# Performance work log

Hardware: AMD Instinct MI355X
Metric: run time of the kernel (lower is better)

Reference implementation:

```python
import jax, jax.numpy as jnp
import numpy as np

N_NODES = 40000
N_EDGES = 640000
MUL = 32                      # multiplicity of 0e and 1o in node irreps
NUM_NEIGHBORS = 16.0
SILU_NORM = 1.6791767923989418  # e3nn normalize2mom factor for silu
SQRT3 = 3.0 ** 0.5


def setup_inputs() -> dict:
    key = jax.random.key(0)
    ks = jax.random.split(key, 12)
    return {
        "node_input": jax.random.normal(ks[0], (N_NODES, 4 * MUL), dtype=jnp.float32),
        "node_attr": jnp.ones((N_NODES, 1), dtype=jnp.float32),
        "edge_src": jax.random.randint(ks[1], (N_EDGES,), 0, N_NODES, dtype=jnp.int32),
        "edge_dst": jax.random.randint(ks[2], (N_EDGES,), 0, N_NODES, dtype=jnp.int32),
        "edge_attr": jax.random.normal(ks[3], (N_EDGES, 4), dtype=jnp.float32),
        "edge_scalars": jax.random.normal(ks[4], (N_EDGES, 8), dtype=jnp.float32),
        "w_lin1_s": jax.random.normal(ks[5], (MUL, MUL), dtype=jnp.float32),
        "w_lin1_v": jax.random.normal(ks[6], (MUL, MUL), dtype=jnp.float32),
        "fc_w1": jax.random.normal(ks[7], (8, 64), dtype=jnp.float32),
        "fc_w2": jax.random.normal(ks[8], (64, 4 * MUL), dtype=jnp.float32),
        "w_lin2_s": jax.random.normal(ks[9], (2 * MUL, MUL), dtype=jnp.float32),
        "w_lin2_v": jax.random.normal(ks[10], (2 * MUL, MUL), dtype=jnp.float32),
    }


def reference(node_input, node_attr, edge_src, edge_dst, edge_attr, edge_scalars,
              w_lin1_s, w_lin1_v, fc_w1, fc_w2, w_lin2_s, w_lin2_v):
    N = node_input.shape[0]
    # split node features per e3nn layout: [32x0e | 32x1o]
    s = node_input[:, :MUL]                            # [N, 32]
    v = node_input[:, MUL:].reshape(N, MUL, 3)         # [N, 32, 3]

    # linear_1: per-irrep e3nn Linear (weights scaled by 1/sqrt(fan_in))
    s = s @ (w_lin1_s / jnp.sqrt(jnp.float32(MUL)))
    v = jnp.einsum('nui,uw->nwi', v, w_lin1_v / jnp.sqrt(jnp.float32(MUL)))

    # fc: edge_scalars -> tensor-product weights (e3nn FullyConnectedNet, silu)
    h = jax.nn.silu(edge_scalars @ (fc_w1 / jnp.sqrt(jnp.float32(fc_w1.shape[0])))) * SILU_NORM
    w = h @ (fc_w2 / jnp.sqrt(jnp.float32(fc_w2.shape[0])))      # [E, 128]
    w0 = w[:, 0 * MUL:1 * MUL]  # path 0e x 0e -> 0e
    w1 = w[:, 1 * MUL:2 * MUL]  # path 0e x 1o -> 1o
    w2 = w[:, 2 * MUL:3 * MUL]  # path 1o x 0e -> 1o
    w3 = w[:, 3 * MUL:4 * MUL]  # path 1o x 1o -> 0e

    # gather source node features per edge
    se = s[edge_src]            # [E, 32]
    ve = v[edge_src]            # [E, 32, 3]
    es = edge_attr[:, :1]       # [E, 1]  edge 0e
    ev = edge_attr[:, 1:4]      # [E, 3]  edge 1o

    # edge-wise 'uvu' Clebsch-Gordan tensor product (e3nn component-normalized;
    # the sqrt(3) path weight cancels the 1/sqrt(3) of w3j for the l=1 paths)
    mid_s0 = w0 * se * es                                       # 0e x 0e -> 0e
    mid_s1 = w3 * jnp.einsum('eui,ei->eu', ve, ev) / SQRT3      # 1o x 1o -> 0e
    mid_v0 = (w1 * se)[:, :, None] * ev[:, None, :]             # 0e x 1o -> 1o
    mid_v1 = (w2 * es)[:, :, None] * ve                         # 1o x 0e -> 1o
    # sorted irreps_mid layout: [0e(path0), 0e(path3) | 1o(path1), 1o(path2)]
    mid_scal = jnp.concatenate([mid_s0, mid_s1], axis=1)        # [E, 64]
    mid_vec = jnp.concatenate([mid_v0, mid_v1], axis=1)         # [E, 64, 3]

    # scatter-reduce to destination nodes, / sqrt(num_neighbors)
    inv = 1.0 / jnp.sqrt(jnp.float32(NUM_NEIGHBORS))
    ns = jax.ops.segment_sum(mid_scal, edge_dst, num_segments=N) * inv   # [N, 64]
    nv = jax.ops.segment_sum(mid_vec, edge_dst, num_segments=N) * inv    # [N, 64, 3]

    # linear_2: 64x0e+64x1o -> 32x0e+32x1o
    fan = jnp.sqrt(jnp.float32(2 * MUL))
    out_s = ns @ (w_lin2_s / fan)                                # [N, 32]
    out_v = jnp.einsum('nui,uw->nwi', nv, w_lin2_v / fan)        # [N, 32, 3]
    return jnp.concatenate([out_s, out_v.reshape(N, -1)], axis=1)
```

## Files before the change

kernel.cpp:

```cpp
#include <hip/hip_runtime.h>
#include <math.h>

#define NNODES 40000
#define NEDGES 640000
#define NPB 8
#define LROW 257
#define CHUNK 32
#define CHUNK4 16
#define MROW 260
#define NB1 8

typedef __attribute__((ext_vector_type(8))) short short8_t;
typedef __attribute__((ext_vector_type(4))) short short4_t;
typedef __attribute__((ext_vector_type(4))) float float4_t;

__device__ __forceinline__ float4 ld4(const float* p) { return *(const float4*)p; }

__device__ __forceinline__ unsigned short bf16r(float x) {
  union { float f; unsigned u; } v; v.f = x;
  unsigned u = v.u;
  u += 0x7FFFu + ((u >> 16) & 1u);
  return (unsigned short)(u >> 16);
}

__device__ __forceinline__ void lds_fadd(float* p, float v) {
  __hip_atomic_fetch_add(p, v, __ATOMIC_RELAXED, __HIP_MEMORY_SCOPE_WORKGROUP);
}

#define INV_SQRT3_C 0.57735026918962576f

__device__ __forceinline__ void accum_half(float* lrow, int u,
    float w0, float w1, float w2, float w3,
    float se, float vx, float vy, float vz,
    float esc, float ev0, float ev1, float ev2) {
  lds_fadd(lrow + u, w0 * se * esc);
  float dv = vx * ev0 + vy * ev1 + vz * ev2;
  lds_fadd(lrow + 32 + u, w3 * dv * INV_SQRT3_C);
  float b1v = w1 * se;
  lds_fadd(lrow + 64 + u * 3 + 0, b1v * ev0);
  lds_fadd(lrow + 64 + u * 3 + 1, b1v * ev1);
  lds_fadd(lrow + 64 + u * 3 + 2, b1v * ev2);
  float b2v = w2 * esc;
  lds_fadd(lrow + 160 + u * 3 + 0, b2v * vx);
  lds_fadd(lrow + 160 + u * 3 + 1, b2v * vy);
  lds_fadd(lrow + 160 + u * 3 + 2, b2v * vz);
}

struct RowData { float se0, se1, vx0, vy0, vz0, vx1, vy1, vz1; };

__device__ __forceinline__ RowData load_row(const float* ab, int m) {
  RowData d;
  d.se0 = ab[m];            d.se1 = ab[m + 16];
  d.vx0 = ab[32 + 3 * m];   d.vy0 = ab[33 + 3 * m];   d.vz0 = ab[34 + 3 * m];
  d.vx1 = ab[80 + 3 * m];   d.vy1 = ab[81 + 3 * m];   d.vz1 = ab[82 + 3 * m];
  return d;
}

__global__ void k1_stage1(const float* __restrict__ node_input,
                          const float* __restrict__ w1s,
                          const float* __restrict__ w1v,
                          float* __restrict__ A) {
  const float scale = 0.17677669529663687f;
  int stride = gridDim.x * blockDim.x;
  for (int idx = blockIdx.x * blockDim.x + threadIdx.x; idx < NNODES * 128; idx += stride) {
    int n = idx >> 7;
    int c = idx & 127;
    const float* row = node_input + n * 128;
    float acc = 0.f;
    if (c < 32) {
      #pragma unroll
      for (int u = 0; u < 32; ++u)
        acc = fmaf(row[u], w1s[u * 32 + c], acc);
    } else {
      int cc = c - 32;
      int w = cc / 3;
      int i = cc - w * 3;
      #pragma unroll
      for (int u = 0; u < 32; ++u)
        acc = fmaf(row[32 + u * 3 + i], w1v[u * 32 + w], acc);
    }
    A[idx] = acc * scale;
  }
}

__global__ __launch_bounds__(256) void k1_stage1b(
    const float* __restrict__ node_input,
    const float* __restrict__ w1s,
    const float* __restrict__ w1v,
    float* __restrict__ A2) {
  __shared__ float rows[NB1 * 128];
  __shared__ float ws[32 * 32];
  __shared__ float wvv[32 * 32];
  const float scale = 0.17677669529663687f;
  int tid = threadIdx.x;
  int n0 = blockIdx.x * NB1;

  float4 a = ((const float4*)w1s)[tid];
  a.x *= scale; a.y *= scale; a.z *= scale; a.w *= scale;
  ((float4*)ws)[tid] = a;
  float4 b = ((const float4*)w1v)[tid];
  b.x *= scale; b.y *= scale; b.z *= scale; b.w *= scale;
  ((float4*)wvv)[tid] = b;
  ((float4*)rows)[tid] = ((const float4*)(node_input + (long)n0 * 128))[tid];
  __syncthreads();

  int j = tid & 31, g = tid >> 5;
  const float* lr = rows + g * 128;
  float ac0 = 0.f, ac1 = 0.f, ac2 = 0.f, ac3 = 0.f;
  #pragma unroll
  for (int t = 0; t < 32; ++t) {
    float wsj = ws[t * 32 + j];
    float wvj = wvv[t * 32 + j];
    ac0 = fmaf(lr[t],            wsj, ac0);
    ac1 = fmaf(lr[32 + 3 * t],     wvj, ac1);
    ac2 = fmaf(lr[32 + 3 * t + 1], wvj, ac2);
    ac3 = fmaf(lr[32 + 3 * t + 2], wvj, ac3);
  }
  float4 o; o.x = ac0; o.y = ac1; o.z = ac2; o.w = ac3;
  ((float4*)(A2 + (long)n0 * 128))[tid] = o;
}

__global__ void k_hist(const int* __restrict__ edge_dst, int* __restrict__ counts) {
  int e = blockIdx.x * blockDim.x + threadIdx.x;
  if (e < NEDGES) atomicAdd(&counts[edge_dst[e]], 1);
}

__global__ void k_scanA(const int* __restrict__ counts, int* __restrict__ bsum) {
  __shared__ int ws[4];
  int t = blockIdx.x * 256 + threadIdx.x;
  int v = (t < NNODES) ? counts[t] : 0;
  for (int d = 32; d; d >>= 1) v += __shfl_down(v, d, 64);
  if ((threadIdx.x & 63) == 0) ws[threadIdx.x >> 6] = v;
  __syncthreads();
  if (threadIdx.x == 0) bsum[blockIdx.x] = ws[0] + ws[1] + ws[2] + ws[3];
}

__global__ __launch_bounds__(256) void k_scanB(const int* __restrict__ bsum,
                                               int* __restrict__ boff,
                                               int* __restrict__ offsets) {
  __shared__ int s[256];
  int tid = threadIdx.x;
  int v = (tid < 157) ? bsum[tid] : 0;
  s[tid] = v;
  __syncthreads();
  for (int d = 1; d < 256; d <<= 1) {
    int x = (tid >= d) ? s[tid - d] : 0;
    __syncthreads();
    s[tid] += x;
    __syncthreads();
  }
  if (tid < 157) boff[tid] = s[tid] - v;
  if (tid == 0) offsets[NNODES] = NEDGES;
}

__global__ __launch_bounds__(256) void k_scanC(const int* __restrict__ counts,
                                               const int* __restrict__ boff,
                                               int* __restrict__ offsets,
                                               int* __restrict__ cursor) {
  __shared__ int s[256];
  int tid = threadIdx.x;
  int t = blockIdx.x * 256 + tid;
  int v = (t < NNODES) ? counts[t] : 0;
  s[tid] = v;
  __syncthreads();
  for (int d = 1; d < 256; d <<= 1) {
    int x = (tid >= d) ? s[tid - d] : 0;
    __syncthreads();
    s[tid] += x;
    __syncthreads();
  }
  int off = boff[blockIdx.x] + s[tid] - v;
  if (t < NNODES) { offsets[t] = off; cursor[t] = off; }
}

__global__ __launch_bounds__(256) void k_scanBC(
    const int* __restrict__ counts,
    const int* __restrict__ bsum,
    int* __restrict__ offsets,
    int* __restrict__ cursor) {
  __shared__ int sb[256];
  __shared__ int s[256];
  int tid = threadIdx.x;
  int vb = (tid < 157) ? bsum[tid] : 0;
  sb[tid] = vb;
  __syncthreads();
  for (int d = 1; d < 256; d <<= 1) {
    int x = (tid >= d) ? sb[tid - d] : 0;
    __syncthreads();
    sb[tid] += x;
    __syncthreads();
  }
  int myboff = (blockIdx.x == 0) ? 0 : sb[blockIdx.x - 1];
  int t = blockIdx.x * 256 + tid;
  int v = (t < NNODES) ? counts[t] : 0;
  s[tid] = v;
  __syncthreads();
  for (int d = 1; d < 256; d <<= 1) {
    int x = (tid >= d) ? s[tid - d] : 0;
    __syncthreads();
    s[tid] += x;
    __syncthreads();
  }
  int off = myboff + s[tid] - v;
  if (t < NNODES) { offsets[t] = off; cursor[t] = off; }
  if (blockIdx.x == 0 && tid == 0) offsets[NNODES] = NEDGES;
}

__global__ void k_scatter(const int* __restrict__ edge_dst,
                          int* __restrict__ cursor, int* __restrict__ slots) {
  int e = blockIdx.x * blockDim.x + threadIdx.x;
  if (e < NEDGES) {
    int d = edge_dst[e];
    int p = atomicAdd(&cursor[d], 1);
    slots[p] = e;
  }
}

__global__ void k_scatter_pack2(const int* __restrict__ edge_src,
                                const int* __restrict__ edge_dst,
                                const float* __restrict__ edge_attr,
                                const float* __restrict__ edge_scalars,
                                int* __restrict__ cursor,
                                int* __restrict__ PSRC,
                                float4_t* __restrict__ PEA,
                                float4_t* __restrict__ PES) {
  int e = blockIdx.x * blockDim.x + threadIdx.x;
  if (e < NEDGES) {
    int d = edge_dst[e];
    int p = atomicAdd(&cursor[d], 1);
    PSRC[p] = edge_src[e];
    PEA[p] = *(const float4_t*)(edge_attr + (long)e * 4);
    PES[2 * p]     = *(const float4_t*)(edge_scalars + (long)e * 8);
    PES[2 * p + 1] = *(const float4_t*)(edge_scalars + (long)e * 8 + 4);
  }
}

__global__ void k_scatter_pack3(const int* __restrict__ edge_src,
                                const int* __restrict__ edge_dst,
                                const float* __restrict__ edge_attr,
                                const float* __restrict__ edge_scalars,
                                int* __restrict__ cursor,
                                float4_t* __restrict__ PE) {
  int e = blockIdx.x * blockDim.x + threadIdx.x;
  if (e < NEDGES) {
    int d = edge_dst[e];
    int p = atomicAdd(&cursor[d], 1);
    float4_t* b = PE + (long)p * 4;
    b[0] = *(const float4_t*)(edge_attr + (long)e * 4);
    b[1] = *(const float4_t*)(edge_scalars + (long)e * 8);
    b[2] = *(const float4_t*)(edge_scalars + (long)e * 8 + 4);
    float4_t s;
    s.x = __int_as_float(edge_src[e]); s.y = 0.f; s.z = 0.f; s.w = 0.f;
    b[3] = s;
  }
}

__global__ __launch_bounds__(256, 4) void k_edge6(
    const float* __restrict__ A2,
    const float4_t* __restrict__ PE,
    const float* __restrict__ fc_w1,
    const float* __restrict__ fc_w2,
    const float* __restrict__ w2s,
    const float* __restrict__ w2v,
    const int* __restrict__ offsets,
    float* __restrict__ out) {
  const float INV_SQRT8 = 0.35355339059327373f;
  const float H_SCALE   = 1.6791767923989418f / 8.0f;
  const float S2SCALE   = 0.03125f;

  __shared__ float  mid[CHUNK4 * MROW];
  __shared__ short  h_lds[CHUNK4 * 72];
  __shared__ float4 w1f[144];

  int tid = threadIdx.x;
  int n0 = blockIdx.x * NPB;
  int ebase = offsets[n0];
  int eend  = offsets[n0 + NPB];

  if (tid < 128) {
    int j = tid >> 1, hf = tid & 1;
    float4 wv4;
    wv4.x = fc_w1[(hf * 4 + 0) * 64 + j] * INV_SQRT8;
    wv4.y = fc_w1[(hf * 4 + 1) * 64 + j] * INV_SQRT8;
    wv4.z = fc_w1[(hf * 4 + 2) * 64 + j] * INV_SQRT8;
    wv4.w = fc_w1[(hf * 4 + 3) * 64 + j] * INV_SQRT8;
    w1f[(j >> 3) * 18 + (j & 7) * 2 + hf] = wv4;
  }

  int wv = tid >> 6;
  int l  = tid & 63;
// ... 11 lines not shown
    bL0[j] = (short)bf16r(fc_w2[(q * 8 + j) * 128      + tL * 16 + m]);
    bL1[j] = (short)bf16r(fc_w2[(32 + q * 8 + j) * 128 + tL * 16 + m]);
    bH0[j] = (short)bf16r(fc_w2[(q * 8 + j) * 128      + tH * 16 + m]);
    bH1[j] = (short)bf16r(fc_w2[(32 + q * 8 + j) * 128 + tH * 16 + m]);
  }

  int nA = 2 * wv;
  int offA0 = offsets[n0 + nA];
  int offA1 = offsets[n0 + nA + 1];
  int offB1 = offsets[n0 + nA + 2];
  float4_t racA = {0.f, 0.f, 0.f, 0.f};
  float4_t racB = {0.f, 0.f, 0.f, 0.f};

  float ea0x, ea0y, ea0z, ea0w, ea1x, ea1y, ea1z, ea1w,
        ea2x, ea2y, ea2z, ea2w, ea3x, ea3y, ea3z, ea3w;
  float se0, se1, se2, se3, vx0, vx1, vx2, vx3,
        vy0, vy1, vy2, vy3, vz0, vz1, vz2, vz3;

  auto loadmeta = [&](int kb) {
    int ecs = kb + m;
    int ecc = (ecs < eend) ? ecs : (eend - 1);
    const float4_t* pb = PE + (long)ecc * 4;
    float4_t sA  = pb[1];
    float4_t sB  = pb[2];
    int g  = wv * 2 + (q >> 1);
    int ob = (q & 1) * 4;
    short4_t hq;
    #pragma unroll
    for (int j = 0; j < 4; ++j) {
      float4 wA = w1f[g * 18 + (ob + j) * 2 + 0];
      float4 wB = w1f[g * 18 + (ob + j) * 2 + 1];
      float x = sA.x * wA.x + sA.y * wA.y + sA.z * wA.z + sA.w * wA.w
              + sB.x * wB.x + sB.y * wB.y + sB.z * wB.z + sB.w * wB.w;
      float hv = (x * H_SCALE) / (1.f + __expf(-x));
      hq[j] = (short)bf16r(hv);
    }
    *(short4_t*)((char*)h_lds + m * 144 + wv * 32 + q * 8) = hq;
    int eb = kb + q * 4;
    int e0 = (eb     < eend) ? eb     : (eend - 1);
    int e1 = (eb + 1 < eend) ? eb + 1 : (eend - 1);
    int e2 = (eb + 2 < eend) ? eb + 2 : (eend - 1);
    int e3 = (eb + 3 < eend) ? eb + 3 : (eend - 1);
    const float4_t* p0 = PE + (long)e0 * 4;
    const float4_t* p1 = PE + (long)e1 * 4;
    const float4_t* p2 = PE + (long)e2 * 4;
    const float4_t* p3 = PE + (long)e3 * 4;
    float4_t a0v = p0[0]; int s0i = __float_as_int(p0[3].x);
    float4_t a1v = p1[0]; int s1i = __float_as_int(p1[3].x);
    float4_t a2v = p2[0]; int s2i = __float_as_int(p2[3].x);
    float4_t a3v = p3[0]; int s3i = __float_as_int(p3[3].x);
    ea0x = a0v.x; ea0y = a0v.y; ea0z = a0v.z; ea0w = a0v.w;
    ea1x = a1v.x; ea1y = a1v.y; ea1z = a1v.z; ea1w = a1v.w;
    ea2x = a2v.x; ea2y = a2v.y; ea2z = a2v.z; ea2w = a2v.w;
    ea3x = a3v.x; ea3y = a3v.y; ea3z = a3v.z; ea3w = a3v.w;
    float4 g0 = *(const float4*)(A2 + (long)s0i * 128 + 4 * u);
    float4 g1 = *(const float4*)(A2 + (long)s1i * 128 + 4 * u);
    float4 g2 = *(const float4*)(A2 + (long)s2i * 128 + 4 * u);
    float4 g3 = *(const float4*)(A2 + (long)s3i * 128 + 4 * u);
    se0 = g0.x; vx0 = g0.y; vy0 = g0.z; vz0 = g0.w;
    se1 = g1.x; vx1 = g1.y; vy1 = g1.z; vz1 = g1.w;
    se2 = g2.x; vx2 = g2.y; vy2 = g2.z; vz2 = g2.w;
    se3 = g3.x; vx3 = g3.y; vy3 = g3.z; vz3 = g3.w;
  };

  __syncthreads();

  if (ebase < eend) {
// ... 44 lines not shown
          float4_t v = *(const float4_t*)(mid + (e - k0) * MROW + 4 * l);
          racB.x += v.x; racB.y += v.y; racB.z += v.z; racB.w += v.w;
        }
      }
      if (k0 + CHUNK4 < eend) loadmeta(k0 + CHUNK4);
    }
  }

  __syncthreads();
  *(float4_t*)(mid + (2 * wv) * MROW + 4 * l)     = racA;
  *(float4_t*)(mid + (2 * wv + 1) * MROW + 4 * l) = racB;
  __syncthreads();
  {
    int j = tid & 31, g = tid >> 5;
    const float* nr = mid + g * MROW;
    float ac0 = 0.f, ac1 = 0.f, ac2 = 0.f, ac3 = 0.f;
    #pragma unroll 8
    for (int t = 0; t < 64; ++t) {
      float wsj = w2s[t * 32 + j];
      float wvj = w2v[t * 32 + j];
      ac0 = fmaf(nr[t],              wsj, ac0);
      ac1 = fmaf(nr[64 + 3 * t],     wvj, ac1);
      ac2 = fmaf(nr[64 + 3 * t + 1], wvj, ac2);
      ac3 = fmaf(nr[64 + 3 * t + 2], wvj, ac3);
    }
    float* po = out + (long)(n0 + g) * 128;
    po[j] = ac0 * S2SCALE;
    po[32 + 3 * j + 0] = ac1 * S2SCALE;
    po[32 + 3 * j + 1] = ac2 * S2SCALE;
    po[32 + 3 * j + 2] = ac3 * S2SCALE;
  }
}

__global__ __launch_bounds__(256, 3) void k_edge3(
    const float* __restrict__ A,
    const int* __restrict__ PSRC,
    const float4_t* __restrict__ PEA,
    const float4_t* __restrict__ PES,
    const float* __restrict__ fc_w1,
    const float* __restrict__ fc_w2,
    const int* __restrict__ offsets,
    float* __restrict__ ACC) {
  const float INV_SQRT8 = 0.35355339059327373f;
  const float H_SCALE   = 1.6791767923989418f / 8.0f;

  __shared__ float    mid[CHUNK * MROW];
  __shared__ short8_t w2frag[16 * 64];
  __shared__ float4   w1f[144];

  int tid = threadIdx.x;
  int n0 = blockIdx.x * NPB;
  int ebase = offsets[n0];
  int eend  = offsets[n0 + NPB];

  if (tid < 128) {
    int j = tid >> 1, hf = tid & 1;
    float4 wv4;
    wv4.x = fc_w1[(hf * 4 + 0) * 64 + j] * INV_SQRT8;
    wv4.y = fc_w1[(hf * 4 + 1) * 64 + j] * INV_SQRT8;
    wv4.z = fc_w1[(hf * 4 + 2) * 64 + j] * INV_SQRT8;
    wv4.w = fc_w1[(hf * 4 + 3) * 64 + j] * INV_SQRT8;
    w1f[(j >> 3) * 18 + (j & 7) * 2 + hf] = wv4;
  }
  for (int fi = tid; fi < 16 * 64; fi += 256) {
    int f = fi >> 6, ll = fi & 63;
    int ct = f >> 1, kh = f & 1, mm = ll & 15, qq = ll >> 4;
    short8_t v;
    #pragma unroll
    for (int j = 0; j < 8; ++j)
      v[j] = (short)bf16r(fc_w2[(kh * 32 + qq * 8 + j) * 128 + ct * 16 + mm]);
    w2frag[fi] = v;
  }
  __syncthreads();

  int wv = tid >> 6;
  int l  = tid & 63;
  int m  = l & 15;
  int q  = l >> 4;
  int et = wv & 1;
  int ch = wv >> 1;

  int nA = 2 * wv;
  int offA0 = offsets[n0 + nA];
  int offA1 = offsets[n0 + nA + 1];
  int offB1 = offsets[n0 + nA + 2];
  float4_t racA = {0.f, 0.f, 0.f, 0.f};
  float4_t racB = {0.f, 0.f, 0.f, 0.f};

  for (int k0 = ebase; k0 < eend; k0 += CHUNK) {
    {
      int ecs = k0 + et * 16 + m;
      int ecc = (ecs < eend) ? ecs : (eend - 1);
      int srcm = PSRC[ecc];
      float4 eam = *(const float4*)(PEA + ecc);
      float4 sA  = *(const float4*)(PES + 2 * (long)ecc);
      float4 sB  = *(const float4*)(PES + 2 * (long)ecc + 1);
      float es0 = sA.x, es1 = sA.y, es2 = sA.z, es3 = sA.w;
      float es4 = sB.x, es5 = sB.y, es6 = sB.z, es7 = sB.w;

      short8_t a0, a1;
      #pragma unroll
      for (int jj = 0; jj < 8; ++jj) {
        float4 wA = w1f[q * 18 + jj * 2 + 0];
        float4 wB = w1f[q * 18 + jj * 2 + 1];
        float x = es0 * wA.x + es1 * wA.y + es2 * wA.z + es3 * wA.w
                + es4 * wB.x + es5 * wB.y + es6 * wB.z + es7 * wB.w;
        float hv = (x * H_SCALE) / (1.f + __expf(-x));
        a0[jj] = (short)bf16r(hv);
        float4 wC = w1f[(4 + q) * 18 + jj * 2 + 0];
        float4 wD = w1f[(4 + q) * 18 + jj * 2 + 1];
        float x2 = es0 * wC.x + es1 * wC.y + es2 * wC.z + es3 * wC.w
                 + es4 * wD.x + es5 * wD.y + es6 * wD.z + es7 * wD.w;
        float hv2 = (x2 * H_SCALE) / (1.f + __expf(-x2));
        a1[jj] = (short)bf16r(hv2);
      }

      int sl0 = q * 4, sl1 = sl0 + 1, sl2 = sl0 + 2, sl3 = sl0 + 3;
      int src0 = __shfl(srcm, sl0, 64), src1 = __shfl(srcm, sl1, 64);
      int src2 = __shfl(srcm, sl2, 64), src3 = __shfl(srcm, sl3, 64);
      float ea0x = __shfl(eam.x, sl0, 64), ea0y = __shfl(eam.y, sl0, 64),
            ea0z = __shfl(eam.z, sl0, 64), ea0w = __shfl(eam.w, sl0, 64);
      float ea1x = __shfl(eam.x, sl1, 64), ea1y = __shfl(eam.y, sl1, 64),
            ea1z = __shfl(eam.z, sl1, 64), ea1w = __shfl(eam.w, sl1, 64);
      float ea2x = __shfl(eam.x, sl2, 64), ea2y = __shfl(eam.y, sl2, 64),
            ea2z = __shfl(eam.z, sl2, 64), ea2w = __shfl(eam.w, sl2, 64);
      float ea3x = __shfl(eam.x, sl3, 64), ea3y = __shfl(eam.y, sl3, 64),
            ea3z = __shfl(eam.z, sl3, 64), ea3w = __shfl(eam.w, sl3, 64);

      RowData d0 = load_row(A + (long)src0 * 128, m);
      RowData d1 = load_row(A + (long)src1 * 128, m);
      RowData d2 = load_row(A + (long)src2 * 128, m);
      RowData d3 = load_row(A + (long)src3 * 128, m);

      float4_t acL[2], acH[2];
      #pragma unroll
      for (int uo = 0; uo < 2; ++uo) {
        int tl = ch * 2 + uo;
        short8_t bl0 = w2frag[(tl * 2 + 0) * 64 + l];
        short8_t bl1 = w2frag[(tl * 2 + 1) * 64 + l];
        float4_t zl = (float4_t){0.f, 0.f, 0.f, 0.f};
        zl = __builtin_amdgcn_mfma_f32_16x16x32_bf16(a0, bl0, zl, 0, 0, 0);
        zl = __builtin_amdgcn_mfma_f32_16x16x32_bf16(a1, bl1, zl, 0, 0, 0);
        acL[uo] = zl;
        int th = 4 + ch * 2 + uo;
        short8_t bh0 = w2frag[(th * 2 + 0) * 64 + l];
        short8_t bh1 = w2frag[(th * 2 + 1) * 64 + l];
        float4_t zh = (float4_t){0.f, 0.f, 0.f, 0.f};
        zh = __builtin_amdgcn_mfma_f32_16x16x32_bf16(a0, bh0, zh, 0, 0, 0);
        zh = __builtin_amdgcn_mfma_f32_16x16x32_bf16(a1, bh1, zh, 0, 0, 0);
        acH[uo] = zh;
      }

#define EPI(R, D, EAX, EAY, EAZ, EAW) do {                                       \
        float* mrow = mid + (et * 16 + q * 4 + (R)) * MROW;                      \
        { float wAa = acL[0][R], wBb = acH[0][R];                                \
          if (ch == 0) {                                                         \
            mrow[m] = wAa * D.se0 * EAX;                                         \
            float b = wBb * EAX;                                                 \
            mrow[160 + 3 * m + 0] = b * D.vx0;                                   \
            mrow[160 + 3 * m + 1] = b * D.vy0;                                   \
            mrow[160 + 3 * m + 2] = b * D.vz0;                                   \
          } else {                                                               \
            float dv = D.vx0 * EAY + D.vy0 * EAZ + D.vz0 * EAW;                  \
            mrow[32 + m] = wBb * dv * INV_SQRT3_C;                               \
            float b = wAa * D.se0;                                               \
            mrow[64 + 3 * m + 0] = b * EAY;                                      \
            mrow[64 + 3 * m + 1] = b * EAZ;                                      \
            mrow[64 + 3 * m + 2] = b * EAW;                                      \
          } }                                                                    \
        { float wAa = acL[1][R], wBb = acH[1][R];                                \
          int uu = 16 + m;                                                       \
          if (ch == 0) {                                                         \
            mrow[uu] = wAa * D.se1 * EAX;                                        \
            float b = wBb * EAX;                                                 \
            mrow[160 + 3 * uu + 0] = b * D.vx1;                                  \
            mrow[160 + 3 * uu + 1] = b * D.vy1;                                  \
            mrow[160 + 3 * uu + 2] = b * D.vz1;                                  \
          } else {                                                               \
            float dv = D.vx1 * EAY + D.vy1 * EAZ + D.vz1 * EAW;                  \
            mrow[32 + uu] = wBb * dv * INV_SQRT3_C;                              \
            float b = wAa * D.se1;                                               \
            mrow[64 + 3 * uu + 0] = b * EAY;                                     \
            mrow[64 + 3 * uu + 1] = b * EAZ;                                     \
            mrow[64 + 3 * uu + 2] = b * EAW;                                     \
          } }                                                                    \
      } while (0)

      EPI(0, d0, ea0x, ea0y, ea0z, ea0w);
      EPI(1, d1, ea1x, ea1y, ea1z, ea1w);
      EPI(2, d2, ea2x, ea2y, ea2z, ea2w);
      EPI(3, d3, ea3x, ea3y, ea3z, ea3w);
#undef EPI
    }
    __syncthreads();

    {
      int lo = (offA0 > k0) ? offA0 : k0;
      int hiA = offA1 < (k0 + CHUNK) ? offA1 : (k0 + CHUNK);
      for (int e = lo; e < hiA; ++e) {
        float4_t v = *(const float4_t*)(mid + (e - k0) * MROW + 4 * l);
        racA.x += v.x; racA.y += v.y; racA.z += v.z; racA.w += v.w;
      }
      int lo2 = (offA1 > k0) ? offA1 : k0;
      int hiB = offB1 < (k0 + CHUNK) ? offB1 : (k0 + CHUNK);
      for (int e = lo2; e < hiB; ++e) {
        float4_t v = *(const float4_t*)(mid + (e - k0) * MROW + 4 * l);
        racB.x += v.x; racB.y += v.y; racB.z += v.z; racB.w += v.w;
      }
    }
    __syncthreads();
  }

  *(float4_t*)(ACC + (long)(n0 + nA) * 256 + 4 * l)     = racA;
  *(float4_t*)(ACC + (long)(n0 + nA + 1) * 256 + 4 * l) = racB;
}

__global__ void k3_stage2(const float* __restrict__ ACC,
                          const float* __restrict__ w2s,
                          const float* __restrict__ w2v,
                          float* __restrict__ out) {
  const float scale = 0.03125f;
  int stride = gridDim.x * blockDim.x;
  for (int idx = blockIdx.x * blockDim.x + threadIdx.x; idx < NNODES * 128; idx += stride) {
    int n = idx >> 7;
    int c = idx & 127;
    const float* row = ACC + (long)n * 256;
    float acc = 0.f;
    if (c < 32) {
      #pragma unroll
      for (int qq = 0; qq < 64; ++qq)
        acc = fmaf(row[qq], w2s[qq * 32 + c], acc);
    } else {
      int cc = c - 32;
      int w = cc / 3;
      int i = cc - w * 3;
      #pragma unroll
      for (int qq = 0; qq < 64; ++qq)
        acc = fmaf(row[64 + qq * 3 + i], w2v[qq * 32 + w], acc);
    }
    out[idx] = acc * scale;
  }
}

extern "C" void kernel_launch(void* const* d_in, const int* in_sizes, int n_in,
                              void* d_out, int out_size, void* d_ws, size_t ws_size,
                              hipStream_t stream) {
  const float* node_input   = (const float*)d_in[0];
  const int*   edge_src     = (const int*)d_in[2];
  const int*   edge_dst     = (const int*)d_in[3];
  const float* edge_attr    = (const float*)d_in[4];
  const float* edge_scalars = (const float*)d_in[5];
  const float* fc_w1        = (const float*)d_in[8];
  const float* fc_w2        = (const float*)d_in[9];
  const float* w_lin1_s     = (const float*)d_in[6];
  const float* w_lin1_v     = (const float*)d_in[7];
  const float* w_lin2_s     = (const float*)d_in[10];
  const float* w_lin2_v     = (const float*)d_in[11];

  float* out = (float*)d_out;

  const size_t SZ_ACC = (size_t)NNODES * 256 * sizeof(float);
  const size_t SZ_A2  = (size_t)NNODES * 128 * sizeof(float);
  const size_t SZ_PE  = (size_t)NEDGES * 64;
  const size_t SZ_PES = (size_t)NEDGES * 32;
  const size_t SZ_PEA = (size_t)NEDGES * 16;
  const size_t SZ_PSR = (size_t)NEDGES * 4;
  const size_t SZ_CNT = (size_t)NNODES * sizeof(int);
  const size_t SZ_OFF = (size_t)(NNODES + 4) * sizeof(int);
  const size_t need1 = SZ_A2 + SZ_PE + 3 * SZ_CNT + SZ_OFF + 2048;
  const size_t need2 = SZ_ACC + SZ_PES + SZ_PEA + SZ_PSR + 3 * SZ_CNT + SZ_OFF + 2048;

  if (ws_size >= need1) {
    char* p = (char*)d_ws;
    float*    A2  = (float*)p;    p += SZ_A2;
    float4_t* PE  = (float4_t*)p; p += SZ_PE;
    int* counts   = (int*)p;      p += SZ_CNT;
    int* offsets  = (int*)p;      p += SZ_OFF;
    int* cursor   = (int*)p;      p += SZ_CNT;
    int* bsum     = (int*)p;      p += 160 * sizeof(int);

    hipMemsetAsync(counts, 0, SZ_CNT, stream);
    k1_stage1b<<<NNODES / NB1, 256, 0, stream>>>(node_input, w_lin1_s, w_lin1_v, A2);
    k_hist<<<NEDGES / 256, 256, 0, stream>>>(edge_dst, counts);
    k_scanA<<<157, 256, 0, stream>>>(counts, bsum);
    k_scanBC<<<157, 256, 0, stream>>>(counts, bsum, offsets, cursor);
    k_scatter_pack3<<<NEDGES / 256, 256, 0, stream>>>(edge_src, edge_dst, edge_attr,
                                                      edge_scalars, cursor, PE);
    k_edge6<<<NNODES / NPB, 256, 0, stream>>>(A2, PE, fc_w1, fc_w2,
                                              w_lin2_s, w_lin2_v, offsets, out);
  } else if (ws_size >= need2) {
    float* Abuf = out;
    char* p = (char*)d_ws;
    float*    ACC = (float*)p;    p += SZ_ACC;
    float4_t* PES = (float4_t*)p; p += SZ_PES;
    float4_t* PEA = (float4_t*)p; p += SZ_PEA;
    int*      PSRC = (int*)p;     p += SZ_PSR;
    int* counts   = (int*)p;      p += SZ_CNT;
    int* offsets  = (int*)p;      p += SZ_OFF;
    int* cursor   = (int*)p;      p += SZ_CNT;
    int* bsum     = (int*)p;      p += 160 * sizeof(int);
    int* boff     = (int*)p;      p += 160 * sizeof(int);

    hipMemsetAsync(counts, 0, SZ_CNT, stream);
    k1_stage1<<<2048, 256, 0, stream>>>(node_input, w_lin1_s, w_lin1_v, Abuf);
    k_hist<<<NEDGES / 256, 256, 0, stream>>>(edge_dst, counts);
    k_scanA<<<157, 256, 0, stream>>>(counts, bsum);
    k_scanB<<<1, 256, 0, stream>>>(bsum, boff, offsets);
    k_scanC<<<157, 256, 0, stream>>>(counts, boff, offsets, cursor);
    k_scatter_pack2<<<NEDGES / 256, 256, 0, stream>>>(edge_src, edge_dst, edge_attr,
                                                      edge_scalars, cursor, PSRC, PEA, PES);
    k_edge3<<<NNODES / NPB, 256, 0, stream>>>(Abuf, PSRC, PEA, PES, fc_w1, fc_w2,
                                              offsets, ACC);
    k3_stage2<<<2048, 256, 0, stream>>>(ACC, w_lin2_s, w_lin2_v, out);
  } else {
    float* Abuf = out;
    char* p = (char*)d_ws;
    float*    ACC = (float*)p;    p += SZ_ACC;
    int* counts   = (int*)p;      p += SZ_CNT;
    int* offsets  = (int*)p;      p += SZ_OFF;
    int* cursor   = (int*)p;      p += SZ_CNT;
    int* bsum     = (int*)p;      p += 160 * sizeof(int);
    int* boff     = (int*)p;      p += 160 * sizeof(int);
    int* slots    = (int*)p;      p += (size_t)NEDGES * sizeof(int);
    (void)slots; (void)boff;

    hipMemsetAsync(counts, 0, SZ_CNT, stream);
    k1_stage1<<<2048, 256, 0, stream>>>(node_input, w_lin1_s, w_lin1_v, Abuf);
    k_hist<<<NEDGES / 256, 256, 0, stream>>>(edge_dst, counts);
    k_scanA<<<157, 256, 0, stream>>>(counts, bsum);
    k_scanBC<<<157, 256, 0, stream>>>(counts, bsum, offsets, cursor);
    k_scatter<<<NEDGES / 256, 256, 0, stream>>>(edge_dst, cursor, slots);
    k3_stage2<<<2048, 256, 0, stream>>>(ACC, w_lin2_s, w_lin2_v, out);
  }
}
```

Measured before the change: 329.6 us.

## Fuse graph-build preprocessing into one cooperative kernel with grid syncs

Replaces the memset, linear_1, histogram, scan and scatter-pack launches with a single cooperative kernel that uses grid-wide syncs between phases, falling back to the old launch sequence if the cooperative launch fails. The aim is to cut launch overhead and inter-kernel gaps in the preprocessing stage. It also swaps the silu division for a hardware reciprocal and removes the dead workspace-fallback code paths. The trade-off is that a fixed 1024-block grid runs the low-parallelism scan phases on only 157 blocks while the rest sit idle at the grid barriers, and each grid sync has its own cost.

After: 1.045 ms. 217% more time.

```diff
diff --git a/kernel.cpp b/kernel.cpp
--- a/kernel.cpp
+++ b/kernel.cpp
@@ -1,20 +1,20 @@
 #include <hip/hip_runtime.h>
+#include <hip/hip_cooperative_groups.h>
 #include <math.h>
+
+namespace cg = cooperative_groups;
 
 #define NNODES 40000
 #define NEDGES 640000
 #define NPB 8
-#define LROW 257
-#define CHUNK 32
 #define CHUNK4 16
 #define MROW 260
 #define NB1 8
+#define BUILD_GRID 1024
 
 typedef __attribute__((ext_vector_type(8))) short short8_t;
 typedef __attribute__((ext_vector_type(4))) short short4_t;
 typedef __attribute__((ext_vector_type(4))) float float4_t;
-
-__device__ __forceinline__ float4 ld4(const float* p) { return *(const float4*)p; }
 
 __device__ __forceinline__ unsigned short bf16r(float x) {
   union { float f; unsigned u; } v; v.f = x;
@@ -23,63 +23,122 @@
   return (unsigned short)(u >> 16);
 }
 
-__device__ __forceinline__ void lds_fadd(float* p, float v) {
-  __hip_atomic_fetch_add(p, v, __ATOMIC_RELAXED, __HIP_MEMORY_SCOPE_WORKGROUP);
-}
-
 #define INV_SQRT3_C 0.57735026918962576f
 
-__device__ __forceinline__ void accum_half(float* lrow, int u,
-    float w0, float w1, float w2, float w3,
-    float se, float vx, float vy, float vz,
-    float esc, float ev0, float ev1, float ev2) {
-  lds_fadd(lrow + u, w0 * se * esc);
-  float dv = vx * ev0 + vy * ev1 + vz * ev2;
-  lds_fadd(lrow + 32 + u, w3 * dv * INV_SQRT3_C);
-  float b1v = w1 * se;
-  lds_fadd(lrow + 64 + u * 3 + 0, b1v * ev0);
-  lds_fadd(lrow + 64 + u * 3 + 1, b1v * ev1);
-  lds_fadd(lrow + 64 + u * 3 + 2, b1v * ev2);
-  float b2v = w2 * esc;
-  lds_fadd(lrow + 160 + u * 3 + 0, b2v * vx);
-  lds_fadd(lrow + 160 + u * 3 + 1, b2v * vy);
-  lds_fadd(lrow + 160 + u * 3 + 2, b2v * vz);
-}
-
-struct RowData { float se0, se1, vx0, vy0, vz0, vx1, vy1, vz1; };
-
-__device__ __forceinline__ RowData load_row(const float* ab, int m) {
-  RowData d;
-  d.se0 = ab[m];            d.se1 = ab[m + 16];
-  d.vx0 = ab[32 + 3 * m];   d.vy0 = ab[33 + 3 * m];   d.vz0 = ab[34 + 3 * m];
-  d.vx1 = ab[80 + 3 * m];   d.vy1 = ab[81 + 3 * m];   d.vz1 = ab[82 + 3 * m];
-  return d;
-}
-
-__global__ void k1_stage1(const float* __restrict__ node_input,
-                          const float* __restrict__ w1s,
-                          const float* __restrict__ w1v,
-                          float* __restrict__ A) {
-  const float scale = 0.17677669529663687f;
-  int stride = gridDim.x * blockDim.x;
-  for (int idx = blockIdx.x * blockDim.x + threadIdx.x; idx < NNODES * 128; idx += stride) {
-    int n = idx >> 7;
-    int c = idx & 127;
-    const float* row = node_input + n * 128;
-    float acc = 0.f;
-    if (c < 32) {
+__global__ __launch_bounds__(256, 4) void k_build(
+    const float* __restrict__ node_input,
+    const float* __restrict__ w1s,
+    const float* __restrict__ w1v,
+    float* __restrict__ A2,
+    const int* __restrict__ edge_src,
+    const int* __restrict__ edge_dst,
+    const float* __restrict__ edge_attr,
+    const float* __restrict__ edge_scalars,
+    int* __restrict__ counts,
+    int* __restrict__ bsum,
+    int* __restrict__ offsets,
+    int* __restrict__ cursor,
+    float4_t* __restrict__ PE) {
+  cg::grid_group grid = cg::this_grid();
+  __shared__ float rows[NB1 * 128];
+  __shared__ float wsS[32 * 32];
+  __shared__ float wvS[32 * 32];
+  __shared__ int sb[256];
+  __shared__ int s[256];
+  __shared__ int ws4[4];
+
+  int tid = threadIdx.x;
+  int gthread = blockIdx.x * 256 + tid;
+  int gstride = gridDim.x * 256;
+
+  for (int i = gthread; i < NNODES; i += gstride) counts[i] = 0;
+
+  {
+    const float scale = 0.17677669529663687f;
+    float4 a = ((const float4*)w1s)[tid];
+    a.x *= scale; a.y *= scale; a.z *= scale; a.w *= scale;
+    ((float4*)wsS)[tid] = a;
+    float4 b = ((const float4*)w1v)[tid];
+    b.x *= scale; b.y *= scale; b.z *= scale; b.w *= scale;
+    ((float4*)wvS)[tid] = b;
+    int j = tid & 31, g = tid >> 5;
+    for (int vb = blockIdx.x; vb < NNODES / NB1; vb += gridDim.x) {
+      int n0 = vb * NB1;
+      __syncthreads();
+      ((float4*)rows)[tid] = ((const float4*)(node_input + (long)n0 * 128))[tid];
+      __syncthreads();
+      const float* lr = rows + g * 128;
+      float ac0 = 0.f, ac1 = 0.f, ac2 = 0.f, ac3 = 0.f;
       #pragma unroll
-      for (int u = 0; u < 32; ++u)
-        acc = fmaf(row[u], w1s[u * 32 + c], acc);
-    } else {
-      int cc = c - 32;
-      int w = cc / 3;
-      int i = cc - w * 3;
-      #pragma unroll
-      for (int u = 0; u < 32; ++u)
-        acc = fmaf(row[32 + u * 3 + i], w1v[u * 32 + w], acc);
-    }
-    A[idx] = acc * scale;
+      for (int t = 0; t < 32; ++t) {
+        float wsj = wsS[t * 32 + j];
+        float wvj = wvS[t * 32 + j];
+        ac0 = fmaf(lr[t],              wsj, ac0);
+        ac1 = fmaf(lr[32 + 3 * t],     wvj, ac1);
+        ac2 = fmaf(lr[32 + 3 * t + 1], wvj, ac2);
+        ac3 = fmaf(lr[32 + 3 * t + 2], wvj, ac3);
+      }
+      float4 o; o.x = ac0; o.y = ac1; o.z = ac2; o.w = ac3;
+      ((float4*)(A2 + (long)n0 * 128))[tid] = o;
+    }
+  }
+  __threadfence();
+  grid.sync();
+
+  for (int e = gthread; e < NEDGES; e += gstride)
+    atomicAdd(&counts[edge_dst[e]], 1);
+  __threadfence();
+  grid.sync();
+
+  if (blockIdx.x < 157) {
+    int t = blockIdx.x * 256 + tid;
+    int v = (t < NNODES) ? counts[t] : 0;
+    for (int d = 32; d; d >>= 1) v += __shfl_down(v, d, 64);
+    if ((tid & 63) == 0) ws4[tid >> 6] = v;
+    __syncthreads();
+    if (tid == 0) bsum[blockIdx.x] = ws4[0] + ws4[1] + ws4[2] + ws4[3];
+  }
+  __threadfence();
+  grid.sync();
+
+  if (blockIdx.x < 157) {
+    int vb = (tid < 157) ? bsum[tid] : 0;
+    sb[tid] = vb;
+    __syncthreads();
+    for (int d = 1; d < 256; d <<= 1) {
+      int x = (tid >= d) ? sb[tid - d] : 0;
+      __syncthreads();
+      sb[tid] += x;
+      __syncthreads();
+    }
+    int myboff = (blockIdx.x == 0) ? 0 : sb[blockIdx.x - 1];
+    int t = blockIdx.x * 256 + tid;
+    int v = (t < NNODES) ? counts[t] : 0;
+    s[tid] = v;
+    __syncthreads();
+    for (int d = 1; d < 256; d <<= 1) {
+      int x = (tid >= d) ? s[tid - d] : 0;
+      __syncthreads();
+      s[tid] += x;
+      __syncthreads();
+    }
+    int off = myboff + s[tid] - v;
+    if (t < NNODES) { offsets[t] = off; cursor[t] = off; }
+    if (blockIdx.x == 0 && tid == 0) offsets[NNODES] = NEDGES;
+  }
+  __threadfence();
+  grid.sync();
+
+  for (int e = gthread; e < NEDGES; e += gstride) {
+    int d = edge_dst[e];
+    int p = atomicAdd(&cursor[d], 1);
+    float4_t* b = PE + (long)p * 4;
+    b[0] = *(const float4_t*)(edge_attr + (long)e * 4);
+    b[1] = *(const float4_t*)(edge_scalars + (long)e * 8);
+    b[2] = *(const float4_t*)(edge_scalars + (long)e * 8 + 4);
+    float4_t sv;
+    sv.x = __int_as_float(edge_src[e]); sv.y = 0.f; sv.z = 0.f; sv.w = 0.f;
+    b[3] = sv;
   }
 }
 
@@ -111,7 +170,7 @@
   for (int t = 0; t < 32; ++t) {
     float wsj = ws[t * 32 + j];
     float wvj = wvv[t * 32 + j];
-    ac0 = fmaf(lr[t],            wsj, ac0);
+    ac0 = fmaf(lr[t],              wsj, ac0);
     ac1 = fmaf(lr[32 + 3 * t],     wvj, ac1);
     ac2 = fmaf(lr[32 + 3 * t + 1], wvj, ac2);
     ac3 = fmaf(lr[32 + 3 * t + 2], wvj, ac3);
@@ -133,44 +192,6 @@
   if ((threadIdx.x & 63) == 0) ws[threadIdx.x >> 6] = v;
   __syncthreads();
   if (threadIdx.x == 0) bsum[blockIdx.x] = ws[0] + ws[1] + ws[2] + ws[3];
-}
-
-__global__ __launch_bounds__(256) void k_scanB(const int* __restrict__ bsum,
-                                               int* __restrict__ boff,
-                                               int* __restrict__ offsets) {
-  __shared__ int s[256];
-  int tid = threadIdx.x;
-  int v = (tid < 157) ? bsum[tid] : 0;
-  s[tid] = v;
-  __syncthreads();
-  for (int d = 1; d < 256; d <<= 1) {
-    int x = (tid >= d) ? s[tid - d] : 0;
-    __syncthreads();
-    s[tid] += x;
-    __syncthreads();
-  }
-  if (tid < 157) boff[tid] = s[tid] - v;
-  if (tid == 0) offsets[NNODES] = NEDGES;
-}
-
-__global__ __launch_bounds__(256) void k_scanC(const int* __restrict__ counts,
-                                               const int* __restrict__ boff,
-                                               int* __restrict__ offsets,
-                                               int* __restrict__ cursor) {
-  __shared__ int s[256];
-  int tid = threadIdx.x;
-  int t = blockIdx.x * 256 + tid;
-  int v = (t < NNODES) ? counts[t] : 0;
-  s[tid] = v;
-  __syncthreads();
-  for (int d = 1; d < 256; d <<= 1) {
-    int x = (tid >= d) ? s[tid - d] : 0;
-    __syncthreads();
-    s[tid] += x;
-    __syncthreads();
-  }
-  int off = boff[blockIdx.x] + s[tid] - v;
-  if (t < NNODES) { offsets[t] = off; cursor[t] = off; }
 }
 
 __global__ __launch_bounds__(256) void k_scanBC(
@@ -204,35 +225,6 @@
   int off = myboff + s[tid] - v;
   if (t < NNODES) { offsets[t] = off; cursor[t] = off; }
   if (blockIdx.x == 0 && tid == 0) offsets[NNODES] = NEDGES;
-}
-
-__global__ void k_scatter(const int* __restrict__ edge_dst,
-                          int* __restrict__ cursor, int* __restrict__ slots) {
-  int e = blockIdx.x * blockDim.x + threadIdx.x;
-  if (e < NEDGES) {
-    int d = edge_dst[e];
-    int p = atomicAdd(&cursor[d], 1);
-    slots[p] = e;
-  }
-}
-
-__global__ void k_scatter_pack2(const int* __restrict__ edge_src,
-                                const int* __restrict__ edge_dst,
-                                const float* __restrict__ edge_attr,
-                                const float* __restrict__ edge_scalars,
-                                int* __restrict__ cursor,
-                                int* __restrict__ PSRC,
-                                float4_t* __restrict__ PEA,
-                                float4_t* __restrict__ PES) {
-  int e = blockIdx.x * blockDim.x + threadIdx.x;
-  if (e < NEDGES) {
-    int d = edge_dst[e];
-    int p = atomicAdd(&cursor[d], 1);
-    PSRC[p] = edge_src[e];
-    PEA[p] = *(const float4_t*)(edge_attr + (long)e * 4);
-    PES[2 * p]     = *(const float4_t*)(edge_scalars + (long)e * 8);
-    PES[2 * p + 1] = *(const float4_t*)(edge_scalars + (long)e * 8 + 4);
-  }
 }
 
 __global__ void k_scatter_pack3(const int* __restrict__ edge_src,
@@ -249,13 +241,13 @@
     b[0] = *(const float4_t*)(edge_attr + (long)e * 4);
     b[1] = *(const float4_t*)(edge_scalars + (long)e * 8);
     b[2] = *(const float4_t*)(edge_scalars + (long)e * 8 + 4);
-    float4_t s;
-    s.x = __int_as_float(edge_src[e]); s.y = 0.f; s.z = 0.f; s.w = 0.f;
-    b[3] = s;
-  }
-}
-
-__global__ __launch_bounds__(256, 4) void k_edge6(
+    float4_t sv;
+    sv.x = __int_as_float(edge_src[e]); sv.y = 0.f; sv.z = 0.f; sv.w = 0.f;
+    b[3] = sv;
+  }
+}
+
+__global__ __launch_bounds__(256, 4) void k_edge7(
     const float* __restrict__ A2,
     const float4_t* __restrict__ PE,
     const float* __restrict__ fc_w1,
@@ -333,7 +325,7 @@
       float4 wB = w1f[g * 18 + (ob + j) * 2 + 1];
       float x = sA.x * wA.x + sA.y * wA.y + sA.z * wA.z + sA.w * wA.w
               + sB.x * wB.x + sB.y * wB.y + sB.z * wB.z + sB.w * wB.w;
-      float hv = (x * H_SCALE) / (1.f + __expf(-x));
+      float hv = (x * H_SCALE) * __builtin_amdgcn_rcpf(1.f + __expf(-x));
       hq[j] = (short)bf16r(hv);
     }
     *(short4_t*)((char*)h_lds + m * 144 + wv * 32 + q * 8) = hq;
@@ -444,216 +436,6 @@
   }
 }
 
-__global__ __launch_bounds__(256, 3) void k_edge3(
-    const float* __restrict__ A,
-    const int* __restrict__ PSRC,
-    const float4_t* __restrict__ PEA,
-    const float4_t* __restrict__ PES,
-    const float* __restrict__ fc_w1,
-    const float* __restrict__ fc_w2,
-    const int* __restrict__ offsets,
-    float* __restrict__ ACC) {
-  const float INV_SQRT8 = 0.35355339059327373f;
-  const float H_SCALE   = 1.6791767923989418f / 8.0f;
-
-  __shared__ float    mid[CHUNK * MROW];
-  __shared__ short8_t w2frag[16 * 64];
-  __shared__ float4   w1f[144];
-
-  int tid = threadIdx.x;
-  int n0 = blockIdx.x * NPB;
-  int ebase = offsets[n0];
-  int eend  = offsets[n0 + NPB];
-
-  if (tid < 128) {
-    int j = tid >> 1, hf = tid & 1;
-    float4 wv4;
-    wv4.x = fc_w1[(hf * 4 + 0) * 64 + j] * INV_SQRT8;
-    wv4.y = fc_w1[(hf * 4 + 1) * 64 + j] * INV_SQRT8;
-    wv4.z = fc_w1[(hf * 4 + 2) * 64 + j] * INV_SQRT8;
-    wv4.w = fc_w1[(hf * 4 + 3) * 64 + j] * INV_SQRT8;
-    w1f[(j >> 3) * 18 + (j & 7) * 2 + hf] = wv4;
-  }
-  for (int fi = tid; fi < 16 * 64; fi += 256) {
-    int f = fi >> 6, ll = fi & 63;
-    int ct = f >> 1, kh = f & 1, mm = ll & 15, qq = ll >> 4;
-    short8_t v;
-    #pragma unroll
-    for (int j = 0; j < 8; ++j)
-      v[j] = (short)bf16r(fc_w2[(kh * 32 + qq * 8 + j) * 128 + ct * 16 + mm]);
-    w2frag[fi] = v;
-  }
-  __syncthreads();
-
-  int wv = tid >> 6;
-  int l  = tid & 63;
-  int m  = l & 15;
-  int q  = l >> 4;
-  int et = wv & 1;
-  int ch = wv >> 1;
-
-  int nA = 2 * wv;
-  int offA0 = offsets[n0 + nA];
-  int offA1 = offsets[n0 + nA + 1];
-  int offB1 = offsets[n0 + nA + 2];
-  float4_t racA = {0.f, 0.f, 0.f, 0.f};
-  float4_t racB = {0.f, 0.f, 0.f, 0.f};
-
-  for (int k0 = ebase; k0 < eend; k0 += CHUNK) {
-    {
-      int ecs = k0 + et * 16 + m;
-      int ecc = (ecs < eend) ? ecs : (eend - 1);
-      int srcm = PSRC[ecc];
-      float4 eam = *(const float4*)(PEA + ecc);
-      float4 sA  = *(const float4*)(PES + 2 * (long)ecc);
-      float4 sB  = *(const float4*)(PES + 2 * (long)ecc + 1);
-      float es0 = sA.x, es1 = sA.y, es2 = sA.z, es3 = sA.w;
-      float es4 = sB.x, es5 = sB.y, es6 = sB.z, es7 = sB.w;
-
-      short8_t a0, a1;
-      #pragma unroll
-      for (int jj = 0; jj < 8; ++jj) {
-        float4 wA = w1f[q * 18 + jj * 2 + 0];
-        float4 wB = w1f[q * 18 + jj * 2 + 1];
-        float x = es0 * wA.x + es1 * wA.y + es2 * wA.z + es3 * wA.w
-                + es4 * wB.x + es5 * wB.y + es6 * wB.z + es7 * wB.w;
-        float hv = (x * H_SCALE) / (1.f + __expf(-x));
-        a0[jj] = (short)bf16r(hv);
-        float4 wC = w1f[(4 + q) * 18 + jj * 2 + 0];
-        float4 wD = w1f[(4 + q) * 18 + jj * 2 + 1];
-        float x2 = es0 * wC.x + es1 * wC.y + es2 * wC.z + es3 * wC.w
-                 + es4 * wD.x + es5 * wD.y + es6 * wD.z + es7 * wD.w;
-        float hv2 = (x2 * H_SCALE) / (1.f + __expf(-x2));
-        a1[jj] = (short)bf16r(hv2);
-      }
-
-      int sl0 = q * 4, sl1 = sl0 + 1, sl2 = sl0 + 2, sl3 = sl0 + 3;
-      int src0 = __shfl(srcm, sl0, 64), src1 = __shfl(srcm, sl1, 64);
-      int src2 = __shfl(srcm, sl2, 64), src3 = __shfl(srcm, sl3, 64);
-      float ea0x = __shfl(eam.x, sl0, 64), ea0y = __shfl(eam.y, sl0, 64),
-            ea0z = __shfl(eam.z, sl0, 64), ea0w = __shfl(eam.w, sl0, 64);
-      float ea1x = __shfl(eam.x, sl1, 64), ea1y = __shfl(eam.y, sl1, 64),
-            ea1z = __shfl(eam.z, sl1, 64), ea1w = __shfl(eam.w, sl1, 64);
-      float ea2x = __shfl(eam.x, sl2, 64), ea2y = __shfl(eam.y, sl2, 64),
-            ea2z = __shfl(eam.z, sl2, 64), ea2w = __shfl(eam.w, sl2, 64);
-      float ea3x = __shfl(eam.x, sl3, 64), ea3y = __shfl(eam.y, sl3, 64),
-            ea3z = __shfl(eam.z, sl3, 64), ea3w = __shfl(eam.w, sl3, 64);
-
-      RowData d0 = load_row(A + (long)src0 * 128, m);
-      RowData d1 = load_row(A + (long)src1 * 128, m);
-      RowData d2 = load_row(A + (long)src2 * 128, m);
-      RowData d3 = load_row(A + (long)src3 * 128, m);
-
-      float4_t acL[2], acH[2];
-      #pragma unroll
-      for (int uo = 0; uo < 2; ++uo) {
-        int tl = ch * 2 + uo;
-        short8_t bl0 = w2frag[(tl * 2 + 0) * 64 + l];
-        short8_t bl1 = w2frag[(tl * 2 + 1) * 64 + l];
-        float4_t zl = (float4_t){0.f, 0.f, 0.f, 0.f};
-        zl = __builtin_amdgcn_mfma_f32_16x16x32_bf16(a0, bl0, zl, 0, 0, 0);
-        zl = __builtin_amdgcn_mfma_f32_16x16x32_bf16(a1, bl1, zl, 0, 0, 0);
-        acL[uo] = zl;
-        int th = 4 + ch * 2 + uo;
-        short8_t bh0 = w2frag[(th * 2 + 0) * 64 + l];
-        short8_t bh1 = w2frag[(th * 2 + 1) * 64 + l];
-        float4_t zh = (float4_t){0.f, 0.f, 0.f, 0.f};
-        zh = __builtin_amdgcn_mfma_f32_16x16x32_bf16(a0, bh0, zh, 0, 0, 0);
-        zh = __builtin_amdgcn_mfma_f32_16x16x32_bf16(a1, bh1, zh, 0, 0, 0);
-        acH[uo] = zh;
-      }
-
-#define EPI(R, D, EAX, EAY, EAZ, EAW) do {                                       \
-        float* mrow = mid + (et * 16 + q * 4 + (R)) * MROW;                      \
-        { float wAa = acL[0][R], wBb = acH[0][R];                                \
-          if (ch == 0) {                                                         \
-            mrow[m] = wAa * D.se0 * EAX;                                         \
-            float b = wBb * EAX;                                                 \
-            mrow[160 + 3 * m + 0] = b * D.vx0;                                   \
-            mrow[160 + 3 * m + 1] = b * D.vy0;                                   \
-            mrow[160 + 3 * m + 2] = b * D.vz0;                                   \
-          } else {                                                               \
-            float dv = D.vx0 * EAY + D.vy0 * EAZ + D.vz0 * EAW;                  \
-            mrow[32 + m] = wBb * dv * INV_SQRT3_C;                               \
-            float b = wAa * D.se0;                                               \
-            mrow[64 + 3 * m + 0] = b * EAY;                                      \
-            mrow[64 + 3 * m + 1] = b * EAZ;                                      \
-            mrow[64 + 3 * m + 2] = b * EAW;                                      \
-          } }                                                                    \
-        { float wAa = acL[1][R], wBb = acH[1][R];                                \
-          int uu = 16 + m;                                                       \
-          if (ch == 0) {                                                         \
-            mrow[uu] = wAa * D.se1 * EAX;                                        \
-            float b = wBb * EAX;                                                 \
-            mrow[160 + 3 * uu + 0] = b * D.vx1;                                  \
-            mrow[160 + 3 * uu + 1] = b * D.vy1;                                  \
-            mrow[160 + 3 * uu + 2] = b * D.vz1;                                  \
-          } else {                                                               \
-            float dv = D.vx1 * EAY + D.vy1 * EAZ + D.vz1 * EAW;                  \
-            mrow[32 + uu] = wBb * dv * INV_SQRT3_C;                              \
-            float b = wAa * D.se1;                                               \
-            mrow[64 + 3 * uu + 0] = b * EAY;                                     \
-            mrow[64 + 3 * uu + 1] = b * EAZ;                                     \
-            mrow[64 + 3 * uu + 2] = b * EAW;                                     \
-          } }                                                                    \
-      } while (0)
-
-      EPI(0, d0, ea0x, ea0y, ea0z, ea0w);
-      EPI(1, d1, ea1x, ea1y, ea1z, ea1w);
-      EPI(2, d2, ea2x, ea2y, ea2z, ea2w);
-      EPI(3, d3, ea3x, ea3y, ea3z, ea3w);
-#undef EPI
-    }
-    __syncthreads();
-
-    {
-      int lo = (offA0 > k0) ? offA0 : k0;
-      int hiA = offA1 < (k0 + CHUNK) ? offA1 : (k0 + CHUNK);
-      for (int e = lo; e < hiA; ++e) {
-        float4_t v = *(const float4_t*)(mid + (e - k0) * MROW + 4 * l);
-        racA.x += v.x; racA.y += v.y; racA.z += v.z; racA.w += v.w;
-      }
-      int lo2 = (offA1 > k0) ? offA1 : k0;
-      int hiB = offB1 < (k0 + CHUNK) ? offB1 : (k0 + CHUNK);
-      for (int e = lo2; e < hiB; ++e) {
-        float4_t v = *(const float4_t*)(mid + (e - k0) * MROW + 4 * l);
-        racB.x += v.x; racB.y += v.y; racB.z += v.z; racB.w += v.w;
-      }
-    }
-    __syncthreads();
-  }
-
-  *(float4_t*)(ACC + (long)(n0 + nA) * 256 + 4 * l)     = racA;
-  *(float4_t*)(ACC + (long)(n0 + nA + 1) * 256 + 4 * l) = racB;
-}
-
-__global__ void k3_stage2(const float* __restrict__ ACC,
-                          const float* __restrict__ w2s,
-                          const float* __restrict__ w2v,
-                          float* __restrict__ out) {
-  const float scale = 0.03125f;
-  int stride = gridDim.x * blockDim.x;
-  for (int idx = blockIdx.x * blockDim.x + threadIdx.x; idx < NNODES * 128; idx += stride) {
-    int n = idx >> 7;
-    int c = idx & 127;
-    const float* row = ACC + (long)n * 256;
-    float acc = 0.f;
-    if (c < 32) {
-      #pragma unroll
-      for (int qq = 0; qq < 64; ++qq)
-        acc = fmaf(row[qq], w2s[qq * 32 + c], acc);
-    } else {
-      int cc = c - 32;
-      int w = cc / 3;
-      int i = cc - w * 3;
-      #pragma unroll
-      for (int qq = 0; qq < 64; ++qq)
-        acc = fmaf(row[64 + qq * 3 + i], w2v[qq * 32 + w], acc);
-    }
-    out[idx] = acc * scale;
-  }
-}
-
 extern "C" void kernel_launch(void* const* d_in, const int* in_sizes, int n_in,
                               void* d_out, int out_size, void* d_ws, size_t ws_size,
                               hipStream_t stream) {
@@ -662,35 +444,40 @@
   const int*   edge_dst     = (const int*)d_in[3];
   const float* edge_attr    = (const float*)d_in[4];
   const float* edge_scalars = (const float*)d_in[5];
+  const float* w_lin1_s     = (const float*)d_in[6];
+  const float* w_lin1_v     = (const float*)d_in[7];
   const float* fc_w1        = (const float*)d_in[8];
   const float* fc_w2        = (const float*)d_in[9];
-  const float* w_lin1_s     = (const float*)d_in[6];
-  const float* w_lin1_v     = (const float*)d_in[7];
   const float* w_lin2_s     = (const float*)d_in[10];
   const float* w_lin2_v     = (const float*)d_in[11];
 
   float* out = (float*)d_out;
 
-  const size_t SZ_ACC = (size_t)NNODES * 256 * sizeof(float);
   const size_t SZ_A2  = (size_t)NNODES * 128 * sizeof(float);
   const size_t SZ_PE  = (size_t)NEDGES * 64;
-  const size_t SZ_PES = (size_t)NEDGES * 32;
-  const size_t SZ_PEA = (size_t)NEDGES * 16;
-  const size_t SZ_PSR = (size_t)NEDGES * 4;
   const size_t SZ_CNT = (size_t)NNODES * sizeof(int);
   const size_t SZ_OFF = (size_t)(NNODES + 4) * sizeof(int);
-  const size_t need1 = SZ_A2 + SZ_PE + 3 * SZ_CNT + SZ_OFF + 2048;
-  const size_t need2 = SZ_ACC + SZ_PES + SZ_PEA + SZ_PSR + 3 * SZ_CNT + SZ_OFF + 2048;
-
-  if (ws_size >= need1) {
-    char* p = (char*)d_ws;
-    float*    A2  = (float*)p;    p += SZ_A2;
-    float4_t* PE  = (float4_t*)p; p += SZ_PE;
-    int* counts   = (int*)p;      p += SZ_CNT;
-    int* offsets  = (int*)p;      p += SZ_OFF;
-    int* cursor   = (int*)p;      p += SZ_CNT;
-    int* bsum     = (int*)p;      p += 160 * sizeof(int);
-
+
+  char* p = (char*)d_ws;
+  float*    A2  = (float*)p;    p += SZ_A2;
+  float4_t* PE  = (float4_t*)p; p += SZ_PE;
+  int* counts   = (int*)p;      p += SZ_CNT;
+  int* offsets  = (int*)p;      p += SZ_OFF;
+  int* cursor   = (int*)p;      p += SZ_CNT;
+  int* bsum     = (int*)p;      p += 160 * sizeof(int);
+
+  const float* ni = node_input; const float* w1sp = w_lin1_s; const float* w1vp = w_lin1_v;
+  const int* esp = edge_src; const int* edp = edge_dst;
+  const float* eap = edge_attr; const float* escp = edge_scalars;
+  void* kargs[] = {
+    (void*)&ni, (void*)&w1sp, (void*)&w1vp, (void*)&A2,
+    (void*)&esp, (void*)&edp, (void*)&eap, (void*)&escp,
+    (void*)&counts, (void*)&bsum, (void*)&offsets, (void*)&cursor, (void*)&PE
+  };
+  hipError_t cerr = hipLaunchCooperativeKernel(
+      (const void*)k_build, dim3(BUILD_GRID), dim3(256), kargs, 0, stream);
+  if (cerr != hipSuccess) {
+    (void)hipGetLastError();
     hipMemsetAsync(counts, 0, SZ_CNT, stream);
     k1_stage1b<<<NNODES / NB1, 256, 0, stream>>>(node_input, w_lin1_s, w_lin1_v, A2);
     k_hist<<<NEDGES / 256, 256, 0, stream>>>(edge_dst, counts);
@@ -698,50 +485,8 @@
     k_scanBC<<<157, 256, 0, stream>>>(counts, bsum, offsets, cursor);
     k_scatter_pack3<<<NEDGES / 256, 256, 0, stream>>>(edge_src, edge_dst, edge_attr,
                                                       edge_scalars, cursor, PE);
-    k_edge6<<<NNODES / NPB, 256, 0, stream>>>(A2, PE, fc_w1, fc_w2,
-                                              w_lin2_s, w_lin2_v, offsets, out);
-  } else if (ws_size >= need2) {
-    float* Abuf = out;
-    char* p = (char*)d_ws;
-    float*    ACC = (float*)p;    p += SZ_ACC;
-    float4_t* PES = (float4_t*)p; p += SZ_PES;
-    float4_t* PEA = (float4_t*)p; p += SZ_PEA;
-    int*      PSRC = (int*)p;     p += SZ_PSR;
-    int* counts   = (int*)p;      p += SZ_CNT;
-    int* offsets  = (int*)p;      p += SZ_OFF;
-    int* cursor   = (int*)p;      p += SZ_CNT;
-    int* bsum     = (int*)p;      p += 160 * sizeof(int);
-    int* boff     = (int*)p;      p += 160 * sizeof(int);
-
-    hipMemsetAsync(counts, 0, SZ_CNT, stream);
-    k1_stage1<<<2048, 256, 0, stream>>>(node_input, w_lin1_s, w_lin1_v, Abuf);
-    k_hist<<<NEDGES / 256, 256, 0, stream>>>(edge_dst, counts);
-    k_scanA<<<157, 256, 0, stream>>>(counts, bsum);
-    k_scanB<<<1, 256, 0, stream>>>(bsum, boff, offsets);
-    k_scanC<<<157, 256, 0, stream>>>(counts, boff, offsets, cursor);
-    k_scatter_pack2<<<NEDGES / 256, 256, 0, stream>>>(edge_src, edge_dst, edge_attr,
-                                                      edge_scalars, cursor, PSRC, PEA, PES);
-    k_edge3<<<NNODES / NPB, 256, 0, stream>>>(Abuf, PSRC, PEA, PES, fc_w1, fc_w2,
-                                              offsets, ACC);
-    k3_stage2<<<2048, 256, 0, stream>>>(ACC, w_lin2_s, w_lin2_v, out);
-  } else {
-    float* Abuf = out;
-    char* p = (char*)d_ws;
-    float*    ACC = (float*)p;    p += SZ_ACC;
-    int* counts   = (int*)p;      p += SZ_CNT;
-    int* offsets  = (int*)p;      p += SZ_OFF;
-    int* cursor   = (int*)p;      p += SZ_CNT;
-    int* bsum     = (int*)p;      p += 160 * sizeof(int);
-    int* boff     = (int*)p;      p += 160 * sizeof(int);
-    int* slots    = (int*)p;      p += (size_t)NEDGES * sizeof(int);
-    (void)slots; (void)boff;
-
-    hipMemsetAsync(counts, 0, SZ_CNT, stream);
-    k1_stage1<<<2048, 256, 0, stream>>>(node_input, w_lin1_s, w_lin1_v, Abuf);
-    k_hist<<<NEDGES / 256, 256, 0, stream>>>(edge_dst, counts);
-    k_scanA<<<157, 256, 0, stream>>>(counts, bsum);
-    k_scanBC<<<157, 256, 0, stream>>>(counts, bsum, offsets, cursor);
-    k_scatter<<<NEDGES / 256, 256, 0, stream>>>(edge_dst, cursor, slots);
-    k3_stage2<<<2048, 256, 0, stream>>>(ACC, w_lin2_s, w_lin2_v, out);
-  }
-}
+  }
+
+  k_edge7<<<NNODES / NPB, 256, 0, stream>>>(A2, PE, fc_w1, fc_w2,
+                                            w_lin2_s, w_lin2_v, offsets, out);
+}
```
